# Optimization experiments

Measured on AMD Instinct MI355X. Metric: run time of the kernel, lower is better.

The kernel has to match this reference:

```python
import jax, jax.numpy as jnp
import numpy as np

N_NODES = 100000

def setup_inputs() -> dict:
    key = jax.random.key(0)
    k1, k2, k3, k4 = jax.random.split(key, 4)
    E = 1600000
    x = jax.random.normal(k1, (N_NODES, 128), dtype=jnp.float32)
    src = jax.random.randint(k2, (E,), 0, N_NODES, dtype=jnp.int32)
    dst = jax.random.randint(k3, (E,), 0, N_NODES, dtype=jnp.int32)
    W = jax.random.normal(k4, (128, 128), dtype=jnp.float32) * (1.0 / np.sqrt(128.0))
    b = jnp.zeros((128,), dtype=jnp.float32)
    return {"x": x, "src": src, "dst": dst, "W": W, "b": b}

def reference(x, src, dst, W, b):
    # DGL GraphConv, norm='both', allow_zero_in_degree=True
    N = x.shape[0]
    ones = jnp.ones_like(src, dtype=x.dtype)
    out_deg = jax.ops.segment_sum(ones, src, num_segments=N)
    in_deg = jax.ops.segment_sum(ones, dst, num_segments=N)
    out_norm = jnp.power(jnp.clip(out_deg, 1.0), -0.5)  # [N]
    in_norm = jnp.power(jnp.clip(in_deg, 1.0), -0.5)    # [N]
    h = x * out_norm[:, None]                            # [N, d]
    msg = h[src]                                         # [E, d] gather
    agg = jax.ops.segment_sum(msg, dst, num_segments=N)  # [N, d] scatter-sum
    agg = agg * in_norm[:, None]
    return agg @ W + b
```

## Files before the change

kernel.cpp:

```cpp
#include <hip/hip_runtime.h>

#define NFEAT 128
#define BSHIFT 9
#define BNODES 512
#define NBMAX 256
#define BCAP 9216
#define CHUNK 4096

typedef __attribute__((ext_vector_type(8))) short bf16x8;
typedef __attribute__((ext_vector_type(4))) float f32x4;
typedef unsigned short u16;

__device__ inline u16 f2bf(float f) {
    unsigned u = __float_as_uint(f);
    u += 0x7FFF + ((u >> 16) & 1);
    return (u16)(u >> 16);
}
__device__ inline float bf2f(u16 h) {
    return __uint_as_float((unsigned)h << 16);
}

__global__ __launch_bounds__(256)
void deg_kernel(const int* __restrict__ src, int E, int* __restrict__ out_deg) {
    int stride = gridDim.x * 256;
    for (int i = blockIdx.x * 256 + threadIdx.x; i < E; i += stride)
        atomicAdd(&out_deg[src[i]], 1);
}

__global__ __launch_bounds__(512)
void partition_kernel(const int* __restrict__ src, const int* __restrict__ dst, int E,
                      int* __restrict__ cursor, int* __restrict__ packed, int NB) {
    __shared__ int cnt[NBMAX];
    __shared__ int loff[NBMAX];
    __shared__ int gbase[NBMAX];
    __shared__ int sa[NBMAX], sb[NBMAX];
    __shared__ int sortv[CHUNK];
    __shared__ u16 sortb[CHUNK];

    int tid = threadIdx.x;
    if (tid < NBMAX) cnt[tid] = 0;
    __syncthreads();

    int base = blockIdx.x * CHUNK;
    int endj = min(base + CHUNK, E);
    int ccnt = endj - base;

    for (int j = base + tid; j < endj; j += 512)
        atomicAdd(&cnt[dst[j] >> BSHIFT], 1);
    __syncthreads();

    int v = (tid < NBMAX) ? cnt[tid] : 0;
    if (tid < NBMAX) sa[tid] = v;
    __syncthreads();
    int* s = sa; int* t = sb;
    for (int d = 1; d < NBMAX; d <<= 1) {
        if (tid < NBMAX) t[tid] = s[tid] + (tid >= d ? s[tid - d] : 0);
        __syncthreads();
        int* tmp = s; s = t; t = tmp;
    }
    if (tid < NBMAX) {
        int excl = s[tid] - v;
        loff[tid] = excl;
        cnt[tid] = excl;
        gbase[tid] = v ? (tid * BCAP + atomicAdd(&cursor[tid], v)) : 0;
    }
    __syncthreads();

    for (int j = base + tid; j < endj; j += 512) {
        int d_ = dst[j];
        int bkt = d_ >> BSHIFT;
        int pos = atomicAdd(&cnt[bkt], 1);
        sortv[pos] = ((d_ & (BNODES - 1)) << 17) | src[j];
        sortb[pos] = (u16)bkt;
    }
    __syncthreads();

    for (int p = tid; p < ccnt; p += 512) {
        int bkt = sortb[p];
        packed[gbase[bkt] + (p - loff[bkt])] = sortv[p];
    }
}

__global__ void csr_scan_kernel(const int* __restrict__ cursor,
                                int* __restrict__ csr_base, int NB) {
    __shared__ int sa[256], sb[256];
    int tid = threadIdx.x;
    int v = (tid < NB) ? cursor[tid] : 0;
    sa[tid] = v;
    __syncthreads();
    int* s = sa; int* t = sb;
    for (int d = 1; d < 256; d <<= 1) {
        t[tid] = s[tid] + (tid >= d ? s[tid - d] : 0);
        __syncthreads();
        int* tmp = s; s = t; t = tmp;
    }
    if (tid < NB) csr_base[tid] = s[tid] - v;
    if (tid == 255) csr_base[NB] = s[255];
}

__global__ __launch_bounds__(512)
void fill_cast_kernel(const int* __restrict__ packed, const int* __restrict__ cursor,
                      const int* __restrict__ csr_base,
                      int* __restrict__ row_start, float* __restrict__ inorm,
                      int* __restrict__ csr_src,
                      const float* __restrict__ x, const int* __restrict__ out_deg,
                      u16* __restrict__ xh, const float* __restrict__ W,
                      u16* __restrict__ Wt, int N, int E, int NB, int nbc) {
    int bid = blockIdx.x;
    int tid = threadIdx.x;

    if (bid < NB) {
        __shared__ int cnt[BNODES];
        __shared__ int sa[BNODES], sb[BNODES];
        int bkt = bid;
        int node0 = bkt << BSHIFT;
        int nn = min(BNODES, N - node0);
        int beg = bkt * BCAP;
        int ccnt = cursor[bkt];
        int csr0 = csr_base[bkt];

        cnt[tid] = 0;
        __syncthreads();
        for (int i = tid; i < ccnt; i += 512)
            atomicAdd(&cnt[packed[beg + i] >> 17], 1);
        __syncthreads();

        int v = cnt[tid];
        sa[tid] = v;
        __syncthreads();
        int* s = sa; int* t = sb;
        for (int d = 1; d < 512; d <<= 1) {
            t[tid] = s[tid] + (tid >= d ? s[tid - d] : 0);
            __syncthreads();
            int* tmp = s; s = t; t = tmp;
        }
        int excl = s[tid] - v;

        if (tid < nn) {
            row_start[node0 + tid] = csr0 + excl;
            inorm[node0 + tid] = rsqrtf((float)max(v, 1));
        }
        if (bkt == 0 && tid == 0) row_start[N] = E;
        __syncthreads();

        cnt[tid] = csr0 + excl;
        __syncthreads();
        for (int i = tid; i < ccnt; i += 512) {
            int p = packed[beg + i];
            int slot = atomicAdd(&cnt[p >> 17], 1);
            csr_src[slot] = p & 0x1FFFF;
        }
    } else if (bid < NB + nbc) {
        int node0 = (bid - NB) << 7;
        for (int i = tid; i < 128 * 32; i += 512) {
            int r = i >> 5, f4 = i & 31;
            int n = node0 + r;
            if (n >= N) break;
            float sc = rsqrtf((float)max(out_deg[n], 1));
            float4 vv = *reinterpret_cast<const float4*>(&x[(size_t)n * NFEAT + f4 * 4]);
            ushort4 o;
            o.x = f2bf(vv.x * sc); o.y = f2bf(vv.y * sc);
            o.z = f2bf(vv.z * sc); o.w = f2bf(vv.w * sc);
            *reinterpret_cast<ushort4*>(&xh[(size_t)n * NFEAT + f4 * 4]) = o;
        }
    } else {
        for (int i = tid; i < NFEAT * NFEAT; i += 512) {
            int col = i >> 7, k = i & 127;
            Wt[i] = f2bf(W[k * NFEAT + col]);
        }
    }
}

__global__ __launch_bounds__(256)
void agg_bf16_kernel(const u16* __restrict__ xh, const int* __restrict__ csr_src,
                     const int* __restrict__ row_start, const float* __restrict__ inorm,
                     u16* __restrict__ aggh, int N) {
    int node = blockIdx.x * 8 + (threadIdx.x >> 5);
    if (node >= N) return;
    int lf = threadIdx.x & 31;
    int beg = row_start[node];
    int end = row_start[node + 1];
    const ushort4* xr = reinterpret_cast<const ushort4*>(xh);

    float4 acc = make_float4(0.f, 0.f, 0.f, 0.f);
    for (int i = beg; i < end; i += 8) {
        int s[8];
        float m[8];
        #pragma unroll
        for (int u = 0; u < 8; ++u) {
            int j = i + u;
            bool ok = (j < end);
            s[u] = ok ? csr_src[j] : 0;
            m[u] = ok ? 1.f : 0.f;
        }
        ushort4 v[8];
        #pragma unroll
        for (int u = 0; u < 8; ++u)
            v[u] = xr[(size_t)s[u] * 32 + lf];
        #pragma unroll
        for (int u = 0; u < 8; ++u) {
            acc.x = fmaf(m[u], bf2f(v[u].x), acc.x);
            acc.y = fmaf(m[u], bf2f(v[u].y), acc.y);
            acc.z = fmaf(m[u], bf2f(v[u].z), acc.z);
            acc.w = fmaf(m[u], bf2f(v[u].w), acc.w);
        }
    }
    float in_n = inorm[node];
    ushort4 o;
    o.x = f2bf(acc.x * in_n);
    o.y = f2bf(acc.y * in_n);
    o.z = f2bf(acc.z * in_n);
    o.w = f2bf(acc.w * in_n);
    *reinterpret_cast<ushort4*>(aggh + (size_t)node * 256 + lf * 4) = o;
}

__global__ __launch_bounds__(256)
void mm_mfma_kernel(const u16* __restrict__ aggh, float* outp,
                    const u16* __restrict__ Wt, const float* __restrict__ b, int N) {
    __shared__ u16 Al[NFEAT * NFEAT];
    __shared__ u16 Bl[NFEAT * NFEAT];
    int tid = threadIdx.x;
    int r0 = blockIdx.x * 128;

    for (int c = tid; c < 2048; c += 256) {
        int col = c >> 4, sub = c & 15;
        int slot = sub ^ (col & 7);
        *reinterpret_cast<uint4*>(reinterpret_cast<char*>(Bl) + col * 256 + slot * 16) =
            *reinterpret_cast<const uint4*>(reinterpret_cast<const char*>(Wt) + c * 16);
    }
    for (int c = tid; c < 2048; c += 256) {
        int row = c >> 4, sub = c & 15;
        int grow = min(r0 + row, N - 1);
        int slot = sub ^ (row & 7);
        *reinterpret_cast<uint4*>(reinterpret_cast<char*>(Al) + row * 256 + slot * 16) =
            *reinterpret_cast<const uint4*>(reinterpret_cast<const char*>(aggh) +
                                            (size_t)grow * 512 + sub * 16);
    }
    __syncthreads();

    int lane = tid & 63;
    int wave = tid >> 6;
    int wr = wave >> 1, wc = wave & 1;
    int lrow = lane & 15, hi = lane >> 4;

    f32x4 zero = {0.f, 0.f, 0.f, 0.f};
    f32x4 acc[4][4];
    #pragma unroll
    for (int rt = 0; rt < 4; ++rt)
        #pragma unroll
        for (int ct = 0; ct < 4; ++ct) acc[rt][ct] = zero;

    #pragma unroll
    for (int ks = 0; ks < 4; ++ks) {
        int chunk = ks * 4 + hi;
        bf16x8 af[4], bfr[4];
        #pragma unroll
        for (int rt = 0; rt < 4; ++rt) {
            int row = wr * 64 + rt * 16 + lrow;
            af[rt] = *reinterpret_cast<bf16x8*>(reinterpret_cast<char*>(Al) + row * 256 +
                                                ((chunk ^ (row & 7)) * 16));
        }
        #pragma unroll
        for (int ct = 0; ct < 4; ++ct) {
            int col = wc * 64 + ct * 16 + lrow;
            bfr[ct] = *reinterpret_cast<bf16x8*>(reinterpret_cast<char*>(Bl) + col * 256 +
                                                 ((chunk ^ (col & 7)) * 16));
        }
        #pragma unroll
        for (int rt = 0; rt < 4; ++rt)
            #pragma unroll
            for (int ct = 0; ct < 4; ++ct)
                acc[rt][ct] = __builtin_amdgcn_mfma_f32_16x16x32_bf16(af[rt], bfr[ct],
                                                                     acc[rt][ct], 0, 0, 0);
    }

    #pragma unroll
    for (int ct = 0; ct < 4; ++ct) {
        int col = wc * 64 + ct * 16 + lrow;
        float bias = b[col];
        #pragma unroll
        for (int rt = 0; rt < 4; ++rt) {
            int rbase = r0 + wr * 64 + rt * 16 + hi * 4;
            #pragma unroll
            for (int q = 0; q < 4; ++q) {
                int row = rbase + q;
                if (row < N) outp[(size_t)row * NFEAT + col] = acc[rt][ct][q] + bias;
            }
        }
    }
}

extern "C" void kernel_launch(void* const* d_in, const int* in_sizes, int n_in,
                              void* d_out, int out_size, void* d_ws, size_t ws_size,
                              hipStream_t stream) {
    const float* x   = (const float*)d_in[0];
    const int*   src = (const int*)d_in[1];
    const int*   dst = (const int*)d_in[2];
    const float* W   = (const float*)d_in[3];
    const float* b   = (const float*)d_in[4];

    const int N = in_sizes[0] / NFEAT;
    const int E = in_sizes[1];
    float* out = (float*)d_out;

    const int NB = (N + BNODES - 1) >> BSHIFT;

    int*   out_deg   = (int*)d_ws;
    int*   cursor    = out_deg + N;
    int*   csr_base  = cursor + NBMAX;
    int*   row_start = csr_base + (NBMAX + 1);
    float* inorm     = (float*)(row_start + (N + 1));
    int*   csr_src   = (int*)(inorm + N);
    u16*   Wt        = (u16*)(csr_src + E);
    u16*   xh        = Wt + NFEAT * NFEAT;

    int* packed = (int*)d_out;

    hipMemsetAsync(d_ws, 0, (size_t)(N + NBMAX) * sizeof(int), stream);

    deg_kernel<<<2048, 256, 0, stream>>>(src, E, out_deg);

    int nchunk = (E + CHUNK - 1) / CHUNK;
    partition_kernel<<<nchunk, 512, 0, stream>>>(src, dst, E, cursor, packed, NB);
    csr_scan_kernel<<<1, 256, 0, stream>>>(cursor, csr_base, NB);

    int nbc = (N + 127) >> 7;
    fill_cast_kernel<<<NB + nbc + 1, 512, 0, stream>>>(packed, cursor, csr_base,
                                                       row_start, inorm, csr_src,
                                                       x, out_deg, xh, W, Wt, N, E, NB, nbc);

    u16* aggh = (u16*)d_out;
    agg_bf16_kernel<<<(N + 7) / 8, 256, 0, stream>>>(xh, csr_src, row_start, inorm, aggh, N);

    mm_mfma_kernel<<<(N + 127) / 128, 256, 0, stream>>>(aggh, out, Wt, b, N);
}
```

Baseline: 227.5 us.

## Fuse out-degree count into partition and bucket scan into fill kernel

The standalone degree kernel is removed and its atomic out-degree increments move into the partition kernel's first pass, which already reads each edge. The single-block bucket-offset scan kernel is removed and every bucket block in the fill kernel recomputes the 256-entry prefix sum locally. This drops two kernel launches and one extra read of src. In exchange, each fill block does a redundant small scan and the partition pass carries more global atomic traffic.

```diff
diff --git a/kernel.cpp b/kernel.cpp
--- a/kernel.cpp
+++ b/kernel.cpp
@@ -20,16 +20,10 @@
     return __uint_as_float((unsigned)h << 16);
 }
 
-__global__ __launch_bounds__(256)
-void deg_kernel(const int* __restrict__ src, int E, int* __restrict__ out_deg) {
-    int stride = gridDim.x * 256;
-    for (int i = blockIdx.x * 256 + threadIdx.x; i < E; i += stride)
-        atomicAdd(&out_deg[src[i]], 1);
-}
-
 __global__ __launch_bounds__(512)
 void partition_kernel(const int* __restrict__ src, const int* __restrict__ dst, int E,
-                      int* __restrict__ cursor, int* __restrict__ packed, int NB) {
+                      int* __restrict__ cursor, int* __restrict__ packed,
+                      int* __restrict__ out_deg, int NB) {
     __shared__ int cnt[NBMAX];
     __shared__ int loff[NBMAX];
     __shared__ int gbase[NBMAX];
@@ -45,8 +39,10 @@
     int endj = min(base + CHUNK, E);
     int ccnt = endj - base;
 
-    for (int j = base + tid; j < endj; j += 512)
+    for (int j = base + tid; j < endj; j += 512) {
+        atomicAdd(&out_deg[src[j]], 1);
         atomicAdd(&cnt[dst[j] >> BSHIFT], 1);
+    }
     __syncthreads();
 
     int v = (tid < NBMAX) ? cnt[tid] : 0;
@@ -81,26 +77,8 @@
     }
 }
 
-__global__ void csr_scan_kernel(const int* __restrict__ cursor,
-                                int* __restrict__ csr_base, int NB) {
-    __shared__ int sa[256], sb[256];
-    int tid = threadIdx.x;
-    int v = (tid < NB) ? cursor[tid] : 0;
-    sa[tid] = v;
-    __syncthreads();
-    int* s = sa; int* t = sb;
-    for (int d = 1; d < 256; d <<= 1) {
-        t[tid] = s[tid] + (tid >= d ? s[tid - d] : 0);
-        __syncthreads();
-        int* tmp = s; s = t; t = tmp;
-    }
-    if (tid < NB) csr_base[tid] = s[tid] - v;
-    if (tid == 255) csr_base[NB] = s[255];
-}
-
 __global__ __launch_bounds__(512)
 void fill_cast_kernel(const int* __restrict__ packed, const int* __restrict__ cursor,
-                      const int* __restrict__ csr_base,
                       int* __restrict__ row_start, float* __restrict__ inorm,
                       int* __restrict__ csr_src,
                       const float* __restrict__ x, const int* __restrict__ out_deg,
@@ -112,12 +90,23 @@
     if (bid < NB) {
         __shared__ int cnt[BNODES];
         __shared__ int sa[BNODES], sb[BNODES];
+        __shared__ int ca[256], cb[256];
         int bkt = bid;
         int node0 = bkt << BSHIFT;
         int nn = min(BNODES, N - node0);
         int beg = bkt * BCAP;
         int ccnt = cursor[bkt];
-        int csr0 = csr_base[bkt];
+
+        if (tid < 256) ca[tid] = (tid < NB) ? cursor[tid] : 0;
+        __syncthreads();
+        int* p = ca; int* q = cb;
+        for (int d = 1; d < 256; d <<= 1) {
+            if (tid < 256) q[tid] = p[tid] + (tid >= d ? p[tid - d] : 0);
+            __syncthreads();
+            int* tmp = p; p = q; q = tmp;
+        }
+        int csr0 = (bkt > 0) ? p[bkt - 1] : 0;
+        if (bkt == 0 && tid == 0) row_start[N] = p[NB - 1];
 
         cnt[tid] = 0;
         __syncthreads();
@@ -140,15 +129,14 @@
             row_start[node0 + tid] = csr0 + excl;
             inorm[node0 + tid] = rsqrtf((float)max(v, 1));
         }
-        if (bkt == 0 && tid == 0) row_start[N] = E;
         __syncthreads();
 
         cnt[tid] = csr0 + excl;
         __syncthreads();
         for (int i = tid; i < ccnt; i += 512) {
-            int p = packed[beg + i];
-            int slot = atomicAdd(&cnt[p >> 17], 1);
-            csr_src[slot] = p & 0x1FFFF;
+            int pk = packed[beg + i];
+            int slot = atomicAdd(&cnt[pk >> 17], 1);
+            csr_src[slot] = pk & 0x1FFFF;
         }
     } else if (bid < NB + nbc) {
         int node0 = (bid - NB) << 7;
@@ -307,8 +295,7 @@
 
     int*   out_deg   = (int*)d_ws;
     int*   cursor    = out_deg + N;
-    int*   csr_base  = cursor + NBMAX;
-    int*   row_start = csr_base + (NBMAX + 1);
+    int*   row_start = cursor + NBMAX;
     float* inorm     = (float*)(row_start + (N + 1));
     int*   csr_src   = (int*)(inorm + N);
     u16*   Wt        = (u16*)(csr_src + E);
@@ -318,14 +305,11 @@
 
     hipMemsetAsync(d_ws, 0, (size_t)(N + NBMAX) * sizeof(int), stream);
 
-    deg_kernel<<<2048, 256, 0, stream>>>(src, E, out_deg);
-
     int nchunk = (E + CHUNK - 1) / CHUNK;
-    partition_kernel<<<nchunk, 512, 0, stream>>>(src, dst, E, cursor, packed, NB);
-    csr_scan_kernel<<<1, 256, 0, stream>>>(cursor, csr_base, NB);
+    partition_kernel<<<nchunk, 512, 0, stream>>>(src, dst, E, cursor, packed, out_deg, NB);
 
     int nbc = (N + 127) >> 7;
-    fill_cast_kernel<<<NB + nbc + 1, 512, 0, stream>>>(packed, cursor, csr_base,
+    fill_cast_kernel<<<NB + nbc + 1, 512, 0, stream>>>(packed, cursor,
                                                        row_start, inorm, csr_src,
                                                        x, out_deg, xh, W, Wt, N, E, NB, nbc);
 
```

Result: faster. 216.0 us (-5.1%).
